# Optimization experiments

Measured on AMD Instinct MI355X. Metric: run time of the kernel, lower is better.

Reference implementation:

```python
import jax, jax.numpy as jnp
import numpy as np

DIM = 256
NUM_HEADS = 8
WH, WW = 7, 7
N = WH * WW
B_ = 4096
TABLE = (2 * WH - 1) * (2 * WW - 1)  # 169


def _relative_position_index():
    ch, cw = np.meshgrid(np.arange(WH), np.arange(WW), indexing='ij')
    coords = np.stack([ch, cw]).reshape(2, -1)            # [2, N]
    rel = coords[:, :, None] - coords[:, None, :]          # [2, N, N]
    rel = rel.transpose(1, 2, 0)                           # [N, N, 2]
    rel[:, :, 0] += WH - 1
    rel[:, :, 1] += WW - 1
    rel[:, :, 0] *= 2 * WW - 1
    return jnp.asarray(rel.sum(-1), dtype=jnp.int32)       # [N, N]


def setup_inputs() -> dict:
    key = jax.random.key(0)
    ks = jax.random.split(key, 6)
    x = jax.random.normal(ks[0], (B_, N, DIM), dtype=jnp.float32)
    qkv_w = jax.random.normal(ks[1], (3 * DIM, DIM), dtype=jnp.float32) * 0.02
    qkv_b = jnp.zeros((3 * DIM,), dtype=jnp.float32)
    proj_w = jax.random.normal(ks[2], (DIM, DIM), dtype=jnp.float32) * 0.02
    proj_b = jnp.zeros((DIM,), dtype=jnp.float32)
    bias_table = jax.random.normal(ks[3], (TABLE, NUM_HEADS), dtype=jnp.float32) * 0.02
    rel_idx = _relative_position_index()
    return {"x": x, "qkv_w": qkv_w, "qkv_b": qkv_b, "proj_w": proj_w,
            "proj_b": proj_b, "bias_table": bias_table, "rel_idx": rel_idx}


def reference(x, qkv_w, qkv_b, proj_w, proj_b, bias_table, rel_idx):
    B, n, C = x.shape
    hd = C // NUM_HEADS
    scale = hd ** -0.5
    qkv = (jnp.einsum('bnc,oc->bno', x, qkv_w) + qkv_b)
    qkv = qkv.reshape(B, n, 3, NUM_HEADS, hd).transpose(2, 0, 3, 1, 4)
    q, k, v = qkv[0], qkv[1], qkv[2]
    attn = jnp.einsum('bhnd,bhmd->bhnm', q * scale, k)     # [B, H, N, N]
    # relative position bias gather: [N*N, H] -> [H, N, N]
    bias = bias_table[rel_idx.reshape(-1)].reshape(n, n, NUM_HEADS)
    attn = attn + bias.transpose(2, 0, 1)[None]
    attn = jax.nn.softmax(attn, axis=-1)
    out = jnp.einsum('bhnm,bhmd->bnhd', attn, v).reshape(B, n, C)
    out = jnp.einsum('bnc,oc->bno', out, proj_w) + proj_b
    return out
```

## Files before the change

kernel.cpp:

```cpp
#include <hip/hip_runtime.h>
#include <hip/hip_bf16.h>
#include <stdint.h>

#define NTOK 49
#define NH 8
#define NWIN 4096

typedef short bf16x8 __attribute__((ext_vector_type(8)));
typedef float f32x4 __attribute__((ext_vector_type(4)));

__device__ __forceinline__ f32x4 mfma16(bf16x8 a, bf16x8 b, f32x4 c) {
    return __builtin_amdgcn_mfma_f32_16x16x32_bf16(a, b, c, 0, 0, 0);
}
__device__ __forceinline__ bf16x8 ld8s(const unsigned short* p) {
    return *(const bf16x8*)p;
}
__device__ __forceinline__ unsigned int pk2bf(float a, float b) {
    __hip_bfloat162 h = __float22bfloat162_rn(float2{a, b});
    return *reinterpret_cast<unsigned int*>(&h);
}
__device__ __forceinline__ void st4bf(unsigned short* p, float a, float b, float c, float d) {
    uint2 u;
    u.x = pk2bf(a, b);
    u.y = pk2bf(c, d);
    *reinterpret_cast<uint2*>(p) = u;
}
__device__ __forceinline__ bf16x8 pk8(float4 f0, float4 f1) {
    union { bf16x8 v; unsigned int u[4]; } t;
    t.u[0] = pk2bf(f0.x, f0.y);
    t.u[1] = pk2bf(f0.z, f0.w);
    t.u[2] = pk2bf(f1.x, f1.y);
    t.u[3] = pk2bf(f1.z, f1.w);
    return t.v;
}
__device__ __forceinline__ unsigned short f2bf(float f) {
    union { float f; unsigned int u; } v; v.f = f;
    unsigned int r = v.u + 0x7FFFu + ((v.u >> 16) & 1u);
    return (unsigned short)(r >> 16);
}

__global__ void prep_kernel(const float* __restrict__ qkv_w,
                            const float* __restrict__ proj_w,
                            const float* __restrict__ bias_table,
                            const int* __restrict__ rel_idx,
                            unsigned short* __restrict__ wqkv,
                            unsigned short* __restrict__ wproj,
                            float* __restrict__ biasx)
{
    int i0 = blockIdx.x * blockDim.x + threadIdx.x;
    int stride = gridDim.x * blockDim.x;
    for (int t = i0; t < 768 * 256; t += stride) wqkv[t] = f2bf(qkv_w[t]);
    for (int t = i0; t < 256 * 256; t += stride) wproj[t] = f2bf(proj_w[t]);
    for (int t = i0; t < NH * 64 * 64; t += stride) {
        int h = t >> 12;
        int m = (t >> 6) & 63;
        int n = t & 63;
        float v;
        if (n >= NTOK)      v = -1e30f;
        else if (m >= NTOK) v = 0.0f;
        else                v = bias_table[rel_idx[m * NTOK + n] * NH + h];
        biasx[t] = v;
    }
}

__global__ __launch_bounds__(256, 4) void fused_kernel(
    const float* __restrict__ x,
    const float* __restrict__ qkv_b,
    const unsigned short* __restrict__ wqkv,
    const float* __restrict__ biasx,
    const unsigned short* __restrict__ wproj,
    const float* __restrict__ proj_b,
    float* __restrict__ out)
{
    __shared__ unsigned short smem[31744];
    unsigned short* ao = smem;

    const int tid  = threadIdx.x;
    const int wv   = tid >> 6;
    const int lane = tid & 63;
    const int l16  = lane & 15;
    const int lq   = lane >> 4;
    const int w    = blockIdx.x;
    const float scale = 0.17677669529663687f;

    const int wh = wv & 1;
    const int jt = wv >> 1;
    const int qt = wv;

    const float* xw = x + (size_t)w * (NTOK * 256);

    bf16x8 xfr[2][8];
#pragma unroll
    for (int nt = 0; nt < 2; ++nt) {
        int tok = wh * 32 + nt * 16 + l16;
#pragma unroll
        for (int c = 0; c < 8; ++c) {
            if (tok < NTOK) {
                const float* pp = xw + tok * 256 + c * 32 + lq * 8;
                float4 f0 = *(const float4*)pp;
                float4 f1 = *(const float4*)(pp + 4);
                xfr[nt][c] = pk8(f0, f1);
            } else {
                union { bf16x8 v; unsigned int u[4]; } z;
                z.u[0] = z.u[1] = z.u[2] = z.u[3] = 0;
                xfr[nt][c] = z.v;
            }
        }
    }

    auto qkv_stage = [&](int h, int b) {
        unsigned short* qsb = smem + 16896 + b * 7424;
        unsigned short* ksb = qsb + 2560;
        unsigned short* vtb = qsb + 5120;
#pragma unroll
        for (int ti = 0; ti < 3; ++ti) {
            int tl   = jt * 3 + ti;
            int grp  = tl >> 1;
            int sub  = tl & 1;
            int tile = grp * 16 + 2 * h + sub;
            const unsigned short* bptr = wqkv + (size_t)(tile * 16 + l16) * 256 + lq * 8;
            bf16x8 bfr[8];
#pragma unroll
            for (int c = 0; c < 8; ++c) bfr[c] = ld8s(bptr + c * 32);

            f32x4 acc[2];
            { f32x4 z = {0.f,0.f,0.f,0.f}; acc[0] = z; acc[1] = z; }

            if (grp < 2) {
#pragma unroll
                for (int c = 0; c < 8; ++c)
#pragma unroll
                    for (int nt = 0; nt < 2; ++nt)
                        acc[nt] = mfma16(bfr[c], xfr[nt][c], acc[nt]);
                int chb = tile * 16 + lq * 4;
                float4 bv = *(const float4*)(qkv_b + chb);
                int d0 = sub * 16 + lq * 4;
                unsigned short* dst = (grp == 0 ? qsb : ksb) + d0;
                float sc = (grp == 0) ? scale : 1.0f;
#pragma unroll
                for (int nt = 0; nt < 2; ++nt) {
                    int tok = wh * 32 + nt * 16 + l16;
                    st4bf(dst + tok * 40,
                          (acc[nt][0] + bv.x) * sc, (acc[nt][1] + bv.y) * sc,
                          (acc[nt][2] + bv.z) * sc, (acc[nt][3] + bv.w) * sc);
                }
            } else {
#pragma unroll
                for (int c = 0; c < 8; ++c)
#pragma unroll
                    for (int nt = 0; nt < 2; ++nt)
                        acc[nt] = mfma16(xfr[nt][c], bfr[c], acc[nt]);
                int ch = tile * 16 + l16;
                float bv = qkv_b[ch];
                int d = sub * 16 + l16;
                unsigned short* dst = vtb + d * 72;
#pragma unroll
                for (int nt = 0; nt < 2; ++nt) {
                    int tok0 = wh * 32 + nt * 16 + lq * 4;
                    st4bf(dst + tok0, acc[nt][0] + bv, acc[nt][1] + bv,
                                      acc[nt][2] + bv, acc[nt][3] + bv);
                }
            }
        }
    };

    qkv_stage(0, 0);
    __syncthreads();

#pragma unroll 1
    for (int p = 0; p < NH; ++p) {
        const int b = p & 1;
        unsigned short* qsb = smem + 16896 + b * 7424;
        unsigned short* ksb = qsb + 2560;
        unsigned short* vtb = qsb + 5120;

        bf16x8 kf[4];
#pragma unroll
        for (int mt = 0; mt < 4; ++mt)
            kf[mt] = ld8s(&ksb[(mt * 16 + l16) * 40 + lq * 8]);
        bf16x8 qf = ld8s(&qsb[(qt * 16 + l16) * 40 + lq * 8]);

        f32x4 se[4];
#pragma unroll
        for (int mt = 0; mt < 4; ++mt) { f32x4 z = {0.f,0.f,0.f,0.f}; se[mt] = z; }
#pragma unroll
        for (int mt = 0; mt < 4; ++mt)
            se[mt] = mfma16(kf[mt], qf, se[mt]);

        const int q = qt * 16 + l16;
        const float* bh = biasx + (p << 12);
        float lsum = 0.0f;
#pragma unroll
        for (int mt = 0; mt < 4; ++mt) {
            float4 bb = *(const float4*)(bh + q * 64 + mt * 16 + lq * 4);
            float e0 = __expf(se[mt][0] + bb.x);
            float e1 = __expf(se[mt][1] + bb.y);
            float e2 = __expf(se[mt][2] + bb.z);
            float e3 = __expf(se[mt][3] + bb.w);
            se[mt][0] = e0; se[mt][1] = e1;
            se[mt][2] = e2; se[mt][3] = e3;
            lsum += (e0 + e1) + (e2 + e3);
        }
        lsum += __shfl_xor(lsum, 16);
        lsum += __shfl_xor(lsum, 32);
        float rv = 1.0f / lsum;

        unsigned int P0[4], P1[4];
#pragma unroll
        for (int mt = 0; mt < 4; ++mt) {
            P0[mt] = pk2bf(se[mt][0] * rv, se[mt][1] * rv);
            P1[mt] = pk2bf(se[mt][2] * rv, se[mt][3] * rv);
        }
        int srcA = l16 + ((2 * lq) & 3) * 16;
        int srcB = srcA + 16;
        int hi = lq >> 1;
        bf16x8 pf[2];
#pragma unroll
        for (int kc = 0; kc < 2; ++kc) {
            unsigned int a0 = (unsigned int)__shfl((int)P0[2 * kc],     srcA);
            unsigned int a1 = (unsigned int)__shfl((int)P0[2 * kc + 1], srcA);
            unsigned int b0 = (unsigned int)__shfl((int)P1[2 * kc],     srcA);
            unsigned int b1 = (unsigned int)__shfl((int)P1[2 * kc + 1], srcA);
            unsigned int c0 = (unsigned int)__shfl((int)P0[2 * kc],     srcB);
            unsigned int c1 = (unsigned int)__shfl((int)P0[2 * kc + 1], srcB);
            unsigned int d0 = (unsigned int)__shfl((int)P1[2 * kc],     srcB);
            unsigned int d1 = (unsigned int)__shfl((int)P1[2 * kc + 1], srcB);
            union { bf16x8 v; unsigned int u[4]; } t;
            t.u[0] = hi ? a1 : a0;
            t.u[1] = hi ? b1 : b0;
            t.u[2] = hi ? c1 : c0;
            t.u[3] = hi ? d1 : d0;
            pf[kc] = t.v;
        }

        bf16x8 vf[2][2];
#pragma unroll
        for (int kc = 0; kc < 2; ++kc)
#pragma unroll
            for (int mt = 0; mt < 2; ++mt)
                vf[mt][kc] = ld8s(&vtb[(mt * 16 + l16) * 72 + kc * 32 + lq * 8]);

        f32x4 ot[2];
        { f32x4 z = {0.f,0.f,0.f,0.f}; ot[0] = z; ot[1] = z; }
#pragma unroll
        for (int kc = 0; kc < 2; ++kc)
#pragma unroll
            for (int mt = 0; mt < 2; ++mt)
                ot[mt] = mfma16(vf[mt][kc], pf[kc], ot[mt]);

#pragma unroll
        for (int mt = 0; mt < 2; ++mt)
            st4bf(&ao[q * 264 + p * 32 + mt * 16 + lq * 4],
                  ot[mt][0], ot[mt][1], ot[mt][2], ot[mt][3]);

        if (p < NH - 1) qkv_stage(p + 1, b ^ 1);

        __syncthreads();
    }

    bf16x8 af2[4][8];
#pragma unroll
    for (int nt = 0; nt < 4; ++nt)
#pragma unroll
        for (int c = 0; c < 8; ++c)
            af2[nt][c] = ld8s(&ao[(nt * 16 + l16) * 264 + c * 32 + lq * 8]);

#pragma unroll
    for (int t4 = 0; t4 < 4; ++t4) {
        int tile = wv * 4 + t4;
        const unsigned short* wp = wproj + (size_t)(tile * 16 + l16) * 256 + lq * 8;
        bf16x8 wfr[8];
#pragma unroll
        for (int c = 0; c < 8; ++c) wfr[c] = ld8s(wp + c * 32);

        f32x4 acc[4];
#pragma unroll
        for (int i = 0; i < 4; ++i) { f32x4 z = {0.f,0.f,0.f,0.f}; acc[i] = z; }
#pragma unroll
        for (int c = 0; c < 8; ++c)
#pragma unroll
            for (int nt = 0; nt < 4; ++nt)
                acc[nt] = mfma16(wfr[c], af2[nt][c], acc[nt]);

        int chb = tile * 16 + lq * 4;
        float4 pb = *(const float4*)(proj_b + chb);
#pragma unroll
        for (int nt = 0; nt < 4; ++nt) {
            int tok = nt * 16 + l16;
            if (tok < NTOK) {
                float4 o;
                o.x = acc[nt][0] + pb.x;
                o.y = acc[nt][1] + pb.y;
                o.z = acc[nt][2] + pb.z;
                o.w = acc[nt][3] + pb.w;
                *(float4*)(out + ((size_t)w * NTOK + tok) * 256 + chb) = o;
            }
        }
    }
}

extern "C" void kernel_launch(void* const* d_in, const int* in_sizes, int n_in,
                              void* d_out, int out_size, void* d_ws, size_t ws_size,
                              hipStream_t stream) {
    const float* x          = (const float*)d_in[0];
    const float* qkv_w      = (const float*)d_in[1];
    const float* qkv_b      = (const float*)d_in[2];
    const float* proj_w     = (const float*)d_in[3];
    const float* proj_b     = (const float*)d_in[4];
    const float* bias_table = (const float*)d_in[5];
    const int*   rel_idx    = (const int*)d_in[6];
    float* out = (float*)d_out;

    char* ws = (char*)d_ws;
    unsigned short* wqkv  = (unsigned short*)ws;
    unsigned short* wproj = (unsigned short*)(ws + 393216);
    float*          biasx = (float*)(ws + 524288);

    prep_kernel<<<256, 256, 0, stream>>>(qkv_w, proj_w, bias_table, rel_idx,
                                         wqkv, wproj, biasx);
    fused_kernel<<<NWIN, 256, 0, stream>>>(x, qkv_b, wqkv, biasx, wproj,
                                           proj_b, out);
}
```

Baseline: 839.3 us.

## Stage x in LDS, keep attention output in registers for projection

The x tile is now converted to bf16 once into shared memory and read per stage, instead of being held in registers as 16 fragments per lane. The double-buffered Q/K/V staging becomes single-buffered, with a barrier after each head's loads. Each head's attention output is reshuffled in registers into an A-fragment, so the final projection consumes register-resident data and skips the LDS round-trip. It also changes launch bounds to 3 blocks and adds extra LDS reads and barriers per head in exchange for lower register pressure and no overlap between consecutive heads.

```diff
diff --git a/kernel.cpp b/kernel.cpp
--- a/kernel.cpp
+++ b/kernel.cpp
@@ -24,14 +24,6 @@
     u.x = pk2bf(a, b);
     u.y = pk2bf(c, d);
     *reinterpret_cast<uint2*>(p) = u;
-}
-__device__ __forceinline__ bf16x8 pk8(float4 f0, float4 f1) {
-    union { bf16x8 v; unsigned int u[4]; } t;
-    t.u[0] = pk2bf(f0.x, f0.y);
-    t.u[1] = pk2bf(f0.z, f0.w);
-    t.u[2] = pk2bf(f1.x, f1.y);
-    t.u[3] = pk2bf(f1.z, f1.w);
-    return t.v;
 }
 __device__ __forceinline__ unsigned short f2bf(float f) {
     union { float f; unsigned int u; } v; v.f = f;
@@ -63,7 +55,7 @@
     }
 }
 
-__global__ __launch_bounds__(256, 4) void fused_kernel(
+__global__ __launch_bounds__(256, 3) void fused_kernel(
     const float* __restrict__ x,
     const float* __restrict__ qkv_b,
     const unsigned short* __restrict__ wqkv,
@@ -72,8 +64,11 @@
     const float* __restrict__ proj_b,
     float* __restrict__ out)
 {
-    __shared__ unsigned short smem[31744];
-    unsigned short* ao = smem;
+    __shared__ unsigned short smem[24320];
+    unsigned short* xl = smem;
+    unsigned short* qs = smem + 16896;
+    unsigned short* ks = qs + 2560;
+    unsigned short* vt = ks + 2560;
 
     const int tid  = threadIdx.x;
     const int wv   = tid >> 6;
@@ -89,29 +84,17 @@
 
     const float* xw = x + (size_t)w * (NTOK * 256);
 
-    bf16x8 xfr[2][8];
-#pragma unroll
-    for (int nt = 0; nt < 2; ++nt) {
-        int tok = wh * 32 + nt * 16 + l16;
-#pragma unroll
-        for (int c = 0; c < 8; ++c) {
-            if (tok < NTOK) {
-                const float* pp = xw + tok * 256 + c * 32 + lq * 8;
-                float4 f0 = *(const float4*)pp;
-                float4 f1 = *(const float4*)(pp + 4);
-                xfr[nt][c] = pk8(f0, f1);
-            } else {
-                union { bf16x8 v; unsigned int u[4]; } z;
-                z.u[0] = z.u[1] = z.u[2] = z.u[3] = 0;
-                xfr[nt][c] = z.v;
-            }
-        }
+    for (int t = tid; t < 4096; t += 256) {
+        int row = t >> 6;
+        int col = (t & 63) << 2;
+        float4 f;
+        if (row < NTOK) f = *(const float4*)(xw + row * 256 + col);
+        else { f.x = 0.f; f.y = 0.f; f.z = 0.f; f.w = 0.f; }
+        st4bf(&xl[row * 264 + col], f.x, f.y, f.z, f.w);
     }
-
-    auto qkv_stage = [&](int h, int b) {
-        unsigned short* qsb = smem + 16896 + b * 7424;
-        unsigned short* ksb = qsb + 2560;
-        unsigned short* vtb = qsb + 5120;
+    __syncthreads();
+
+    auto stage = [&](int h) {
 #pragma unroll
         for (int ti = 0; ti < 3; ++ti) {
             int tl   = jt * 3 + ti;
@@ -126,16 +109,24 @@
             f32x4 acc[2];
             { f32x4 z = {0.f,0.f,0.f,0.f}; acc[0] = z; acc[1] = z; }
 
+#pragma unroll
+            for (int c = 0; c < 8; ++c) {
+                bf16x8 xb0 = ld8s(&xl[(wh * 32 + l16) * 264 + c * 32 + lq * 8]);
+                bf16x8 xb1 = ld8s(&xl[(wh * 32 + 16 + l16) * 264 + c * 32 + lq * 8]);
+                if (grp < 2) {
+                    acc[0] = mfma16(bfr[c], xb0, acc[0]);
+                    acc[1] = mfma16(bfr[c], xb1, acc[1]);
+                } else {
+                    acc[0] = mfma16(xb0, bfr[c], acc[0]);
+                    acc[1] = mfma16(xb1, bfr[c], acc[1]);
+                }
+            }
+
             if (grp < 2) {
-#pragma unroll
-                for (int c = 0; c < 8; ++c)
-#pragma unroll
-                    for (int nt = 0; nt < 2; ++nt)
-                        acc[nt] = mfma16(bfr[c], xfr[nt][c], acc[nt]);
                 int chb = tile * 16 + lq * 4;
                 float4 bv = *(const float4*)(qkv_b + chb);
                 int d0 = sub * 16 + lq * 4;
-                unsigned short* dst = (grp == 0 ? qsb : ksb) + d0;
+                unsigned short* dst = (grp == 0 ? qs : ks) + d0;
                 float sc = (grp == 0) ? scale : 1.0f;
 #pragma unroll
                 for (int nt = 0; nt < 2; ++nt) {
@@ -145,15 +136,10 @@
                           (acc[nt][2] + bv.z) * sc, (acc[nt][3] + bv.w) * sc);
                 }
             } else {
-#pragma unroll
-                for (int c = 0; c < 8; ++c)
-#pragma unroll
-                    for (int nt = 0; nt < 2; ++nt)
-                        acc[nt] = mfma16(xfr[nt][c], bfr[c], acc[nt]);
                 int ch = tile * 16 + l16;
                 float bv = qkv_b[ch];
                 int d = sub * 16 + l16;
-                unsigned short* dst = vtb + d * 72;
+                unsigned short* dst = vt + d * 72;
 #pragma unroll
                 for (int nt = 0; nt < 2; ++nt) {
                     int tok0 = wh * 32 + nt * 16 + lq * 4;
@@ -164,21 +150,30 @@
         }
     };
 
-    qkv_stage(0, 0);
+    stage(0);
     __syncthreads();
 
-#pragma unroll 1
+    const int q = qt * 16 + l16;
+    const int srcA = l16 + ((2 * lq) & 3) * 16;
+    const int srcB = srcA + 16;
+    const int hi = lq >> 1;
+
+    bf16x8 paf[NH];
+
+#pragma unroll
     for (int p = 0; p < NH; ++p) {
-        const int b = p & 1;
-        unsigned short* qsb = smem + 16896 + b * 7424;
-        unsigned short* ksb = qsb + 2560;
-        unsigned short* vtb = qsb + 5120;
-
         bf16x8 kf[4];
 #pragma unroll
         for (int mt = 0; mt < 4; ++mt)
-            kf[mt] = ld8s(&ksb[(mt * 16 + l16) * 40 + lq * 8]);
-        bf16x8 qf = ld8s(&qsb[(qt * 16 + l16) * 40 + lq * 8]);
+            kf[mt] = ld8s(&ks[(mt * 16 + l16) * 40 + lq * 8]);
+        bf16x8 qf = ld8s(&qs[(qt * 16 + l16) * 40 + lq * 8]);
+        bf16x8 vf[2][2];
+#pragma unroll
+        for (int kc = 0; kc < 2; ++kc)
+#pragma unroll
+            for (int mt = 0; mt < 2; ++mt)
+                vf[mt][kc] = ld8s(&vt[(mt * 16 + l16) * 72 + kc * 32 + lq * 8]);
+        __syncthreads();
 
         f32x4 se[4];
 #pragma unroll
@@ -187,7 +182,6 @@
         for (int mt = 0; mt < 4; ++mt)
             se[mt] = mfma16(kf[mt], qf, se[mt]);
 
-        const int q = qt * 16 + l16;
         const float* bh = biasx + (p << 12);
         float lsum = 0.0f;
 #pragma unroll
@@ -211,9 +205,6 @@
             P0[mt] = pk2bf(se[mt][0] * rv, se[mt][1] * rv);
             P1[mt] = pk2bf(se[mt][2] * rv, se[mt][3] * rv);
         }
-        int srcA = l16 + ((2 * lq) & 3) * 16;
-        int srcB = srcA + 16;
-        int hi = lq >> 1;
         bf16x8 pf[2];
 #pragma unroll
         for (int kc = 0; kc < 2; ++kc) {
@@ -233,13 +224,6 @@
             pf[kc] = t.v;
         }
 
-        bf16x8 vf[2][2];
-#pragma unroll
-        for (int kc = 0; kc < 2; ++kc)
-#pragma unroll
-            for (int mt = 0; mt < 2; ++mt)
-                vf[mt][kc] = ld8s(&vtb[(mt * 16 + l16) * 72 + kc * 32 + lq * 8]);
-
         f32x4 ot[2];
         { f32x4 z = {0.f,0.f,0.f,0.f}; ot[0] = z; ot[1] = z; }
 #pragma unroll
@@ -248,53 +232,54 @@
             for (int mt = 0; mt < 2; ++mt)
                 ot[mt] = mfma16(vf[mt][kc], pf[kc], ot[mt]);
 
-#pragma unroll
-        for (int mt = 0; mt < 2; ++mt)
-            st4bf(&ao[q * 264 + p * 32 + mt * 16 + lq * 4],
-                  ot[mt][0], ot[mt][1], ot[mt][2], ot[mt][3]);
-
-        if (p < NH - 1) qkv_stage(p + 1, b ^ 1);
-
-        __syncthreads();
+        {
+            unsigned int Q0[2], Q1[2];
+#pragma unroll
+            for (int mt = 0; mt < 2; ++mt) {
+                Q0[mt] = pk2bf(ot[mt][0], ot[mt][1]);
+                Q1[mt] = pk2bf(ot[mt][2], ot[mt][3]);
+            }
+            unsigned int a0 = (unsigned int)__shfl((int)Q0[0], srcA);
+            unsigned int a1 = (unsigned int)__shfl((int)Q0[1], srcA);
+            unsigned int b0 = (unsigned int)__shfl((int)Q1[0], srcA);
+            unsigned int b1 = (unsigned int)__shfl((int)Q1[1], srcA);
+            unsigned int c0 = (unsigned int)__shfl((int)Q0[0], srcB);
+            unsigned int c1 = (unsigned int)__shfl((int)Q0[1], srcB);
+            unsigned int d0 = (unsigned int)__shfl((int)Q1[0], srcB);
+            unsigned int d1 = (unsigned int)__shfl((int)Q1[1], srcB);
+            union { bf16x8 v; unsigned int u[4]; } t;
+            t.u[0] = hi ? a1 : a0;
+            t.u[1] = hi ? b1 : b0;
+            t.u[2] = hi ? c1 : c0;
+            t.u[3] = hi ? d1 : d0;
+            paf[p] = t.v;
+        }
+
+        if (p < NH - 1) {
+            stage(p + 1);
+            __syncthreads();
+        }
     }
 
-    bf16x8 af2[4][8];
-#pragma unroll
-    for (int nt = 0; nt < 4; ++nt)
-#pragma unroll
-        for (int c = 0; c < 8; ++c)
-            af2[nt][c] = ld8s(&ao[(nt * 16 + l16) * 264 + c * 32 + lq * 8]);
-
-#pragma unroll
-    for (int t4 = 0; t4 < 4; ++t4) {
-        int tile = wv * 4 + t4;
-        const unsigned short* wp = wproj + (size_t)(tile * 16 + l16) * 256 + lq * 8;
-        bf16x8 wfr[8];
-#pragma unroll
-        for (int c = 0; c < 8; ++c) wfr[c] = ld8s(wp + c * 32);
-
-        f32x4 acc[4];
-#pragma unroll
-        for (int i = 0; i < 4; ++i) { f32x4 z = {0.f,0.f,0.f,0.f}; acc[i] = z; }
-#pragma unroll
-        for (int c = 0; c < 8; ++c)
-#pragma unroll
-            for (int nt = 0; nt < 4; ++nt)
-                acc[nt] = mfma16(wfr[c], af2[nt][c], acc[nt]);
-
-        int chb = tile * 16 + lq * 4;
+    const int tok = qt * 16 + l16;
+#pragma unroll
+    for (int t4 = 0; t4 < 16; ++t4) {
+        const unsigned short* wp = wproj + (size_t)(t4 * 16 + l16) * 256 + lq * 8;
+        f32x4 acc = {0.f, 0.f, 0.f, 0.f};
+#pragma unroll
+        for (int c = 0; c < 8; ++c) {
+            bf16x8 wfr = ld8s(wp + c * 32);
+            acc = mfma16(wfr, paf[c], acc);
+        }
+        int chb = t4 * 16 + lq * 4;
         float4 pb = *(const float4*)(proj_b + chb);
-#pragma unroll
-        for (int nt = 0; nt < 4; ++nt) {
-            int tok = nt * 16 + l16;
-            if (tok < NTOK) {
-                float4 o;
-                o.x = acc[nt][0] + pb.x;
-                o.y = acc[nt][1] + pb.y;
-                o.z = acc[nt][2] + pb.z;
-                o.w = acc[nt][3] + pb.w;
-                *(float4*)(out + ((size_t)w * NTOK + tok) * 256 + chb) = o;
-            }
+        if (tok < NTOK) {
+            float4 o;
+            o.x = acc[0] + pb.x;
+            o.y = acc[1] + pb.y;
+            o.z = acc[2] + pb.z;
+            o.w = acc[3] + pb.w;
+            *(float4*)(out + ((size_t)w * NTOK + tok) * 256 + chb) = o;
         }
     }
 }
```

After: 965.5 us. 15.0% more time.
